# Optimization experiments

Measured on AMD Instinct MI355X. Metric: run time of the kernel, lower is better.

The kernel has to match this reference:

```python
import jax, jax.numpy as jnp
import numpy as np

GRID_W, GRID_H = 4, 4          # num_splits = (4, 4) -> 16 experts
N = 524288                     # number of sample points
IN_DIM, HID, OUT = 2, 256, 3   # per-expert MLP: 2 -> 256 -> 3


def setup_inputs() -> dict:
    key = jax.random.key(0)
    k_s, k_w1, k_w2 = jax.random.split(key, 3)
    E = GRID_W * GRID_H
    samples = jax.random.uniform(k_s, (N, IN_DIM), dtype=jnp.float32)
    W1 = jax.random.normal(k_w1, (E, IN_DIM, HID), dtype=jnp.float32) * (1.0 / np.sqrt(IN_DIM))
    b1 = jnp.zeros((E, HID), dtype=jnp.float32)
    W2 = jax.random.normal(k_w2, (E, HID, OUT), dtype=jnp.float32) * (1.0 / np.sqrt(HID))
    b2 = jnp.zeros((E, OUT), dtype=jnp.float32)
    return {"samples": samples, "W1": W1, "b1": b1, "W2": W2, "b2": b2}


def _grid_inds(samples):
    # i, j = floor(samples[:, d] * n).clip(0, n-1); inds = j * w + i
    i = jnp.clip(jnp.floor(samples[:, 0] * GRID_W), 0, GRID_W - 1)
    j = jnp.clip(jnp.floor(samples[:, 1] * GRID_H), 0, GRID_H - 1)
    return (j * GRID_W + i).astype(jnp.int32)  # [N]


def reference(samples, W1, b1, W2, b2):
    inds = _grid_inds(samples)                     # [N] expert id per sample
    E = W1.shape[0]
    out = jnp.zeros((samples.shape[0], W2.shape[-1]), dtype=samples.dtype)
    # Dense dispatch: loop over the small fixed set of experts (16) and
    # select each sample's own expert output via the routing mask. Same
    # math as torch's features[inds == i] gather + scatter combine.
    for e in range(E):
        h = jax.nn.relu(samples @ W1[e] + b1[e])   # [N, HID]
        y = h @ W2[e] + b2[e]                      # [N, OUT]
        out = jnp.where((inds == e)[:, None], y, out)
    return out
```

## Files before the change

kernel.cpp:

```cpp
#include <hip/hip_runtime.h>

typedef _Float16 h2 __attribute__((ext_vector_type(2)));

#define GRID_W 4
#define GRID_H 4
#define NEXP   16
#define HID    256
#define TPB    1024
#define S      2
#define SAMP   (TPB * S)
#define NWAVE  (TPB / 64)
#define GR     64
#define MAXENT 48

#define NSLOT   (SAMP + GR)
#define OFFB_Y  (NSLOT * 16)
#define OFFB_I  (OFFB_Y + SAMP * 12)
#define LDS_BYTES (OFFB_I + 4 * (16 + 17 + 17 + 3 * MAXENT + 1))

#define WPE_H2  768
#define WSOFF_M2  768
#define WSOFF_MIX 4096

union H8 { float4 f; h2 p[4]; };

__global__ __launch_bounds__(256) void prep_kernel(
    const float* __restrict__ W1, const float* __restrict__ b1,
    const float* __restrict__ W2, const float* __restrict__ b2,
    float* __restrict__ wsAff, int* __restrict__ wsM2,
    _Float16* __restrict__ wsMix) {
    __shared__ float sA[9];
    __shared__ int sCnt;
    __shared__ _Float16 tA[256], tB[256], tC[256], tU0[256], tU1[256], tU2[256];

    const int e = blockIdx.x, k = threadIdx.x;
    if (k < 9) sA[k] = 0.f;
    if (k == 0) sCnt = 0;
    __syncthreads();

    float a  = W1[e * 512 + k];
    float b  = W1[e * 512 + 256 + k];
    float c  = b1[e * 256 + k];
    float u0 = W2[e * 768 + 3 * k];
    float u1 = W2[e * 768 + 3 * k + 1];
    float u2 = W2[e * 768 + 3 * k + 2];

    int ci = e & 3, cj = e >> 2;
    float x0 = ci * 0.25f, x1 = x0 + 0.25f;
    float y0 = cj * 0.25f, y1 = y0 + 0.25f;
    float vmin = fminf(a * x0, a * x1) + fminf(b * y0, b * y1) + c;
    float vmax = fmaxf(a * x0, a * x1) + fmaxf(b * y0, b * y1) + c;

    if (vmin >= 0.f) {
        atomicAdd(&sA[0], u0 * a); atomicAdd(&sA[1], u0 * b); atomicAdd(&sA[2], u0 * c);
        atomicAdd(&sA[3], u1 * a); atomicAdd(&sA[4], u1 * b); atomicAdd(&sA[5], u1 * c);
        atomicAdd(&sA[6], u2 * a); atomicAdd(&sA[7], u2 * b); atomicAdd(&sA[8], u2 * c);
    } else if (vmax > 0.f) {
        int p = atomicAdd(&sCnt, 1);
        tA[p] = (_Float16)a;  tB[p] = (_Float16)b;  tC[p] = (_Float16)c;
        tU0[p] = (_Float16)u0; tU1[p] = (_Float16)u1; tU2[p] = (_Float16)u2;
    }
    __syncthreads();

    int M = sCnt;
    int M2r = (((M + 1) >> 1) + 3) & ~3;
    for (int t = M + k; t < 2 * M2r; t += 256) {
        tA[t] = (_Float16)0.f; tB[t] = (_Float16)0.f; tC[t] = (_Float16)0.f;
        tU0[t] = (_Float16)0.f; tU1[t] = (_Float16)0.f; tU2[t] = (_Float16)0.f;
    }
    __syncthreads();

    h2* dst = (h2*)(wsMix + (size_t)e * (2 * WPE_H2));
    if (k < M2r) {
        h2 v;
        v.x = tA[2 * k];  v.y = tA[2 * k + 1];  dst[k]       = v;
        v.x = tB[2 * k];  v.y = tB[2 * k + 1];  dst[128 + k] = v;
        v.x = tC[2 * k];  v.y = tC[2 * k + 1];  dst[256 + k] = v;
        v.x = tU0[2 * k]; v.y = tU0[2 * k + 1]; dst[384 + k] = v;
        v.x = tU1[2 * k]; v.y = tU1[2 * k + 1]; dst[512 + k] = v;
        v.x = tU2[2 * k]; v.y = tU2[2 * k + 1]; dst[640 + k] = v;
    }
    if (k == 0) {
        wsM2[e] = M2r;
        float* af = wsAff + e * 12;
        af[0] = sA[0]; af[1] = sA[1]; af[2] = b2[3 * e]     + sA[2];
        af[3] = sA[3]; af[4] = sA[4]; af[5] = b2[3 * e + 1] + sA[5];
        af[6] = sA[6]; af[7] = sA[7]; af[8] = b2[3 * e + 2] + sA[8];
        af[9] = 0.f; af[10] = 0.f; af[11] = 0.f;
    }
}

__global__ __launch_bounds__(TPB) void fused_moe_kernel(
    const float2* __restrict__ samples,
    const float* __restrict__ wsAff, const int* __restrict__ wsM2,
    const _Float16* __restrict__ wsMix,
    float* __restrict__ out, int N)
{
    extern __shared__ __align__(16) char smem[];
    int4*  sSlot = (int4*)smem;
    float* sY    = (float*)(smem + OFFB_Y);
    int*   sI    = (int*)(smem + OFFB_I);
    int* sHist = sI;
    int* sOff  = sI + 16;
    int* sES   = sI + 33;
    int* sEexp = sI + 50;
    int* sEbas = sI + 50 + MAXENT;
    int* sEcnt = sI + 50 + 2 * MAXENT;
    int* sC    = sI + 50 + 3 * MAXENT;

    const int tid = threadIdx.x;
    if (tid < NEXP) sHist[tid] = 0;
    __syncthreads();

    const int base0 = blockIdx.x * SAMP;
    float px[S], py[S]; int eid[S], rank[S]; bool act[S];
#pragma unroll
    for (int s = 0; s < S; ++s) {
        int gid = base0 + s * TPB + tid;
        act[s] = gid < N;
        float2 p = act[s] ? samples[gid] : make_float2(0.f, 0.f);
        px[s] = p.x; py[s] = p.y;
        int i = (int)(p.x * (float)GRID_W); i = i < 0 ? 0 : (i > GRID_W - 1 ? GRID_W - 1 : i);
        int j = (int)(p.y * (float)GRID_H); j = j < 0 ? 0 : (j > GRID_H - 1 ? GRID_H - 1 : j);
        eid[s] = j * GRID_W + i;
        rank[s] = act[s] ? atomicAdd(&sHist[eid[s]], 1) : 0;
    }
    __syncthreads();

    if (tid == 0) {
        int acc = 0, ec = 0;
        for (int e = 0; e < NEXP; ++e) {
            sOff[e] = acc; acc += sHist[e];
            sES[e] = ec;  ec  += (sHist[e] + GR - 1) / GR;
        }
        sOff[NEXP] = acc; sES[NEXP] = ec; *sC = ec;
    }
    __syncthreads();

#pragma unroll
    for (int s = 0; s < S; ++s) {
        if (act[s]) {
            int4 v;
            v.x = __float_as_int(px[s]); v.y = __float_as_int(py[s]);
            v.z = s * TPB + tid; v.w = 0;
            sSlot[sOff[eid[s]] + rank[s]] = v;
        }
    }
    int C = *sC;
    if (tid < C) {
        int e = 0;
        while (tid >= sES[e + 1]) ++e;
        int j = tid - sES[e];
        sEexp[tid] = e;
        sEbas[tid] = sOff[e] + j * GR;
        sEcnt[tid] = min(GR, sHist[e] - j * GR);
    }
    __syncthreads();

    const int lane = tid & 63, wv = tid >> 6;
    for (int c = wv; c < C; c += NWAVE) {
        int e   = __builtin_amdgcn_readfirstlane(sEexp[c]);
        int bas = __builtin_amdgcn_readfirstlane(sEbas[c]);
        int cnt = __builtin_amdgcn_readfirstlane(sEcnt[c]);

        int4 v = sSlot[bas + lane];
        float x = __int_as_float(v.x), y = __int_as_float(v.y);
        int ql = v.z;

        const float* af = wsAff + e * 12;
        float y0 = fmaf(x, af[0], fmaf(y, af[1], af[2]));
        float y1 = fmaf(x, af[3], fmaf(y, af[4], af[5]));
        float y2 = fmaf(x, af[6], fmaf(y, af[7], af[8]));

        h2 px2; px2.x = (_Float16)x; px2.y = px2.x;
        h2 py2; py2.x = (_Float16)y; py2.y = py2.x;

        int nb = __builtin_amdgcn_readfirstlane(wsM2[e]) >> 2;
        const float4* Wm = (const float4*)(wsMix + (size_t)e * (2 * WPE_H2));
        for (int bi = 0; bi < nb; ++bi) {
            H8 A, B, Cc, U0, U1, U2;
            A.f  = Wm[bi];        B.f  = Wm[32 + bi];  Cc.f = Wm[64 + bi];
            U0.f = Wm[96 + bi];   U1.f = Wm[128 + bi]; U2.f = Wm[160 + bi];
#pragma unroll
            for (int j = 0; j < 4; ++j) {
                h2 h = __builtin_elementwise_fma(px2, A.p[j],
                       __builtin_elementwise_fma(py2, B.p[j], Cc.p[j]));
                h2 z = (h2)(_Float16)0.0f;
                h = __builtin_elementwise_max(h, z);
#if __has_builtin(__builtin_amdgcn_fdot2)
                y0 = __builtin_amdgcn_fdot2(h, U0.p[j], y0, false);
                y1 = __builtin_amdgcn_fdot2(h, U1.p[j], y1, false);
                y2 = __builtin_amdgcn_fdot2(h, U2.p[j], y2, false);
#else
                y0 += (float)h.x * (float)U0.p[j].x + (float)h.y * (float)U0.p[j].y;
                y1 += (float)h.x * (float)U1.p[j].x + (float)h.y * (float)U1.p[j].y;
                y2 += (float)h.x * (float)U2.p[j].x + (float)h.y * (float)U2.p[j].y;
#endif
            }
        }

        if (lane < cnt) {
            int d = 3 * ql;
            sY[d + 0] = y0; sY[d + 1] = y1; sY[d + 2] = y2;
        }
    }
    __syncthreads();

    int nv = N - base0; if (nv > SAMP) nv = SAMP;
    int dmax = 3 * nv;
    float* outw = out + (size_t)base0 * 3;
#pragma unroll
    for (int r = 0; r < 3 * S; ++r) {
        int d = r * TPB + tid;
        if (d < dmax) outw[d] = sY[d];
    }
}

extern "C" void kernel_launch(void* const* d_in, const int* in_sizes, int n_in,
                              void* d_out, int out_size, void* d_ws, size_t ws_size,
                              hipStream_t stream) {
    const float* samples = (const float*)d_in[0];
    const float* W1      = (const float*)d_in[1];
    const float* b1      = (const float*)d_in[2];
    const float* W2      = (const float*)d_in[3];
    const float* b2      = (const float*)d_in[4];
    float* out = (float*)d_out;

    const int N = in_sizes[0] / 2;
    float*    wsAff = (float*)d_ws;
    int*      wsM2  = (int*)((char*)d_ws + WSOFF_M2);
    _Float16* wsMix = (_Float16*)((char*)d_ws + WSOFF_MIX);

    prep_kernel<<<NEXP, 256, 0, stream>>>(W1, b1, W2, b2, wsAff, wsM2, wsMix);

    const int nblocks = (N + SAMP - 1) / SAMP;
    fused_moe_kernel<<<nblocks, TPB, LDS_BYTES, stream>>>(
        (const float2*)samples, wsAff, wsM2, wsMix, out, N);
}
```

Before: 84.36 us.

## Fold weight-prep kernel into main kernel, building per-expert tables in LDS per block

```diff
diff --git a/kernel.cpp b/kernel.cpp
--- a/kernel.cpp
+++ b/kernel.cpp
@@ -6,100 +6,40 @@
 #define GRID_H 4
 #define NEXP   16
 #define HID    256
-#define TPB    1024
+#define TPB    512
 #define S      2
 #define SAMP   (TPB * S)
 #define NWAVE  (TPB / 64)
 #define GR     64
-#define MAXENT 48
-
-#define NSLOT   (SAMP + GR)
-#define OFFB_Y  (NSLOT * 16)
-#define OFFB_I  (OFFB_Y + SAMP * 12)
-#define LDS_BYTES (OFFB_I + 4 * (16 + 17 + 17 + 3 * MAXENT + 1))
-
-#define WPE_H2  768
-#define WSOFF_M2  768
-#define WSOFF_MIX 4096
+#define MAXENT 33
+
+#define CAPP   120
+#define HPA    (2 * CAPP)
+#define HPE    (6 * HPA)
+#define F4PA   (CAPP / 4)
+#define F4PE   (6 * F4PA)
+
+#define OFFB_AFF  46080
+#define OFFB_SLOT 46848
+#define OFFB_Y    64256
+#define OFFB_I    76544
+#define NSLOT     (SAMP + GR)
+#define LDS_BYTES (OFFB_I + 4 * (16 + 17 + 17 + 3 * MAXENT + 1 + NEXP))
 
 union H8 { float4 f; h2 p[4]; };
 
-__global__ __launch_bounds__(256) void prep_kernel(
-    const float* __restrict__ W1, const float* __restrict__ b1,
-    const float* __restrict__ W2, const float* __restrict__ b2,
-    float* __restrict__ wsAff, int* __restrict__ wsM2,
-    _Float16* __restrict__ wsMix) {
-    __shared__ float sA[9];
-    __shared__ int sCnt;
-    __shared__ _Float16 tA[256], tB[256], tC[256], tU0[256], tU1[256], tU2[256];
-
-    const int e = blockIdx.x, k = threadIdx.x;
-    if (k < 9) sA[k] = 0.f;
-    if (k == 0) sCnt = 0;
-    __syncthreads();
-
-    float a  = W1[e * 512 + k];
-    float b  = W1[e * 512 + 256 + k];
-    float c  = b1[e * 256 + k];
-    float u0 = W2[e * 768 + 3 * k];
-    float u1 = W2[e * 768 + 3 * k + 1];
-    float u2 = W2[e * 768 + 3 * k + 2];
-
-    int ci = e & 3, cj = e >> 2;
-    float x0 = ci * 0.25f, x1 = x0 + 0.25f;
-    float y0 = cj * 0.25f, y1 = y0 + 0.25f;
-    float vmin = fminf(a * x0, a * x1) + fminf(b * y0, b * y1) + c;
-    float vmax = fmaxf(a * x0, a * x1) + fmaxf(b * y0, b * y1) + c;
-
-    if (vmin >= 0.f) {
-        atomicAdd(&sA[0], u0 * a); atomicAdd(&sA[1], u0 * b); atomicAdd(&sA[2], u0 * c);
-        atomicAdd(&sA[3], u1 * a); atomicAdd(&sA[4], u1 * b); atomicAdd(&sA[5], u1 * c);
-        atomicAdd(&sA[6], u2 * a); atomicAdd(&sA[7], u2 * b); atomicAdd(&sA[8], u2 * c);
-    } else if (vmax > 0.f) {
-        int p = atomicAdd(&sCnt, 1);
-        tA[p] = (_Float16)a;  tB[p] = (_Float16)b;  tC[p] = (_Float16)c;
-        tU0[p] = (_Float16)u0; tU1[p] = (_Float16)u1; tU2[p] = (_Float16)u2;
-    }
-    __syncthreads();
-
-    int M = sCnt;
-    int M2r = (((M + 1) >> 1) + 3) & ~3;
-    for (int t = M + k; t < 2 * M2r; t += 256) {
-        tA[t] = (_Float16)0.f; tB[t] = (_Float16)0.f; tC[t] = (_Float16)0.f;
-        tU0[t] = (_Float16)0.f; tU1[t] = (_Float16)0.f; tU2[t] = (_Float16)0.f;
-    }
-    __syncthreads();
-
-    h2* dst = (h2*)(wsMix + (size_t)e * (2 * WPE_H2));
-    if (k < M2r) {
-        h2 v;
-        v.x = tA[2 * k];  v.y = tA[2 * k + 1];  dst[k]       = v;
-        v.x = tB[2 * k];  v.y = tB[2 * k + 1];  dst[128 + k] = v;
-        v.x = tC[2 * k];  v.y = tC[2 * k + 1];  dst[256 + k] = v;
-        v.x = tU0[2 * k]; v.y = tU0[2 * k + 1]; dst[384 + k] = v;
-        v.x = tU1[2 * k]; v.y = tU1[2 * k + 1]; dst[512 + k] = v;
-        v.x = tU2[2 * k]; v.y = tU2[2 * k + 1]; dst[640 + k] = v;
-    }
-    if (k == 0) {
-        wsM2[e] = M2r;
-        float* af = wsAff + e * 12;
-        af[0] = sA[0]; af[1] = sA[1]; af[2] = b2[3 * e]     + sA[2];
-        af[3] = sA[3]; af[4] = sA[4]; af[5] = b2[3 * e + 1] + sA[5];
-        af[6] = sA[6]; af[7] = sA[7]; af[8] = b2[3 * e + 2] + sA[8];
-        af[9] = 0.f; af[10] = 0.f; af[11] = 0.f;
-    }
-}
-
-__global__ __launch_bounds__(TPB) void fused_moe_kernel(
+__global__ __launch_bounds__(TPB, 4) void fused_moe_kernel(
     const float2* __restrict__ samples,
-    const float* __restrict__ wsAff, const int* __restrict__ wsM2,
-    const _Float16* __restrict__ wsMix,
+    const float*  __restrict__ W1, const float* __restrict__ b1,
+    const float*  __restrict__ W2, const float* __restrict__ b2,
     float* __restrict__ out, int N)
 {
     extern __shared__ __align__(16) char smem[];
-    int4*  sSlot = (int4*)smem;
-    float* sY    = (float*)(smem + OFFB_Y);
-    int*   sI    = (int*)(smem + OFFB_I);
+    _Float16* sMix = (_Float16*)smem;
+    float*    sAff = (float*)(smem + OFFB_AFF);
+    int4*     sSlot= (int4*)(smem + OFFB_SLOT);
+    float*    sY   = (float*)(smem + OFFB_Y);
+    int*      sI   = (int*)(smem + OFFB_I);
     int* sHist = sI;
     int* sOff  = sI + 16;
     int* sES   = sI + 33;
@@ -107,8 +47,10 @@
     int* sEbas = sI + 50 + MAXENT;
     int* sEcnt = sI + 50 + 2 * MAXENT;
     int* sC    = sI + 50 + 3 * MAXENT;
+    int* sM2   = sI + 51 + 3 * MAXENT;
 
     const int tid = threadIdx.x;
+    const int lane = tid & 63, wv = tid >> 6;
     if (tid < NEXP) sHist[tid] = 0;
     __syncthreads();
 
@@ -125,13 +67,76 @@
         eid[s] = j * GRID_W + i;
         rank[s] = act[s] ? atomicAdd(&sHist[eid[s]], 1) : 0;
     }
+
+#pragma unroll
+    for (int ee = 0; ee < 2; ++ee) {
+        int e = 2 * wv + ee;
+        float aff[9] = {0.f,0.f,0.f,0.f,0.f,0.f,0.f,0.f,0.f};
+        int basep = 0;
+        _Float16* mb = sMix + e * HPE;
+        int ci = e & 3, cj = e >> 2;
+        float x0 = ci * 0.25f, x1 = x0 + 0.25f;
+        float y0c = cj * 0.25f, y1c = y0c + 0.25f;
+#pragma unroll
+        for (int kc = 0; kc < 4; ++kc) {
+            int k = kc * 64 + lane;
+            float a  = W1[e * 512 + k];
+            float b  = W1[e * 512 + 256 + k];
+            float c  = b1[e * 256 + k];
+            float u0 = W2[e * 768 + 3 * k];
+            float u1 = W2[e * 768 + 3 * k + 1];
+            float u2 = W2[e * 768 + 3 * k + 2];
+            float vmin = fminf(a * x0, a * x1) + fminf(b * y0c, b * y1c) + c;
+            float vmax = fmaxf(a * x0, a * x1) + fmaxf(b * y0c, b * y1c) + c;
+            bool on = vmin >= 0.f;
+            bool mixed = (!on) && (vmax > 0.f);
+            if (on) {
+                aff[0] += u0 * a; aff[1] += u0 * b; aff[2] += u0 * c;
+                aff[3] += u1 * a; aff[4] += u1 * b; aff[5] += u1 * c;
+                aff[6] += u2 * a; aff[7] += u2 * b; aff[8] += u2 * c;
+            }
+            unsigned long long mk = __ballot(mixed);
+            int pos = basep + __popcll(mk & ((1ull << lane) - 1ull));
+            if (mixed && pos < HPA) {
+                mb[pos]           = (_Float16)a;
+                mb[HPA + pos]     = (_Float16)b;
+                mb[2 * HPA + pos] = (_Float16)c;
+                mb[3 * HPA + pos] = (_Float16)u0;
+                mb[4 * HPA + pos] = (_Float16)u1;
+                mb[5 * HPA + pos] = (_Float16)u2;
+            }
+            basep += __popcll(mk);
+        }
+        if (basep > HPA) basep = HPA;
+        int padTo = (basep + 7) & ~7;
+        int idx = basep + lane;
+        if (idx < padTo) {
+            _Float16 z = (_Float16)0.f;
+            mb[idx] = z; mb[HPA + idx] = z; mb[2 * HPA + idx] = z;
+            mb[3 * HPA + idx] = z; mb[4 * HPA + idx] = z; mb[5 * HPA + idx] = z;
+        }
+#pragma unroll
+        for (int j = 0; j < 9; ++j) {
+            float v = aff[j];
+            for (int d = 1; d < 64; d <<= 1) v += __shfl_xor(v, d);
+            aff[j] = v;
+        }
+        if (lane == 0) {
+            float* af = sAff + e * 12;
+            af[0] = aff[0]; af[1] = aff[1]; af[2] = aff[2] + b2[3 * e];
+            af[3] = aff[3]; af[4] = aff[4]; af[5] = aff[5] + b2[3 * e + 1];
+            af[6] = aff[6]; af[7] = aff[7]; af[8] = aff[8] + b2[3 * e + 2];
+            af[9] = 0.f; af[10] = 0.f; af[11] = 0.f;
+            sM2[e] = padTo >> 3;
+        }
+    }
     __syncthreads();
 
     if (tid == 0) {
         int acc = 0, ec = 0;
         for (int e = 0; e < NEXP; ++e) {
             sOff[e] = acc; acc += sHist[e];
-            sES[e] = ec;  ec  += (sHist[e] + GR - 1) / GR;
+            sES[e] = ec;  ec  += (sHist[e] + GR - 1) >> 6;
         }
         sOff[NEXP] = acc; sES[NEXP] = ec; *sC = ec;
     }
@@ -157,7 +162,6 @@
     }
     __syncthreads();
 
-    const int lane = tid & 63, wv = tid >> 6;
     for (int c = wv; c < C; c += NWAVE) {
         int e   = __builtin_amdgcn_readfirstlane(sEexp[c]);
         int bas = __builtin_amdgcn_readfirstlane(sEbas[c]);
@@ -167,7 +171,7 @@
         float x = __int_as_float(v.x), y = __int_as_float(v.y);
         int ql = v.z;
 
-        const float* af = wsAff + e * 12;
+        const float* af = sAff + e * 12;
         float y0 = fmaf(x, af[0], fmaf(y, af[1], af[2]));
         float y1 = fmaf(x, af[3], fmaf(y, af[4], af[5]));
         float y2 = fmaf(x, af[6], fmaf(y, af[7], af[8]));
@@ -175,12 +179,16 @@
         h2 px2; px2.x = (_Float16)x; px2.y = px2.x;
         h2 py2; py2.x = (_Float16)y; py2.y = py2.x;
 
-        int nb = __builtin_amdgcn_readfirstlane(wsM2[e]) >> 2;
-        const float4* Wm = (const float4*)(wsMix + (size_t)e * (2 * WPE_H2));
+        int nb = __builtin_amdgcn_readfirstlane(sM2[e]);
+        const float4* Wm = (const float4*)sMix + e * F4PE;
         for (int bi = 0; bi < nb; ++bi) {
             H8 A, B, Cc, U0, U1, U2;
-            A.f  = Wm[bi];        B.f  = Wm[32 + bi];  Cc.f = Wm[64 + bi];
-            U0.f = Wm[96 + bi];   U1.f = Wm[128 + bi]; U2.f = Wm[160 + bi];
+            A.f  = Wm[bi];
+            B.f  = Wm[F4PA + bi];
+            Cc.f = Wm[2 * F4PA + bi];
+            U0.f = Wm[3 * F4PA + bi];
+            U1.f = Wm[4 * F4PA + bi];
+            U2.f = Wm[5 * F4PA + bi];
 #pragma unroll
             for (int j = 0; j < 4; ++j) {
                 h2 h = __builtin_elementwise_fma(px2, A.p[j],
@@ -227,13 +235,8 @@
     float* out = (float*)d_out;
 
     const int N = in_sizes[0] / 2;
-    float*    wsAff = (float*)d_ws;
-    int*      wsM2  = (int*)((char*)d_ws + WSOFF_M2);
-    _Float16* wsMix = (_Float16*)((char*)d_ws + WSOFF_MIX);
-
-    prep_kernel<<<NEXP, 256, 0, stream>>>(W1, b1, W2, b2, wsAff, wsM2, wsMix);
-
     const int nblocks = (N + SAMP - 1) / SAMP;
+
     fused_moe_kernel<<<nblocks, TPB, LDS_BYTES, stream>>>(
-        (const float2*)samples, wsAff, wsM2, wsMix, out, N);
+        (const float2*)samples, W1, b1, W2, b2, out, N);
 }
```

After: 79.90 us. 1.06x faster.
